# Performance work log

Hardware: AMD Instinct MI355X
Metric: run time of the kernel (lower is better)

Reference implementation:

```python
import jax, jax.numpy as jnp
import numpy as np

B, L, C, K, NLEV, VOCAB, OUT = 32, 1024, 512, 2, 4, 128, 11


def setup_inputs() -> dict:
    key = jax.random.key(0)
    ks = jax.random.split(key, 8)
    x = jax.random.randint(ks[0], (B, L), 0, VOCAB, dtype=jnp.int32)
    mask = jax.random.randint(ks[1], (B, L), 0, 2).astype(jnp.bool_)
    emb = jax.random.uniform(ks[2], (VOCAB, C), minval=-0.5, maxval=0.5, dtype=jnp.float32)
    w1 = jax.random.normal(ks[3], (NLEV, C, C, K), dtype=jnp.float32) * 0.02
    b1 = jnp.zeros((NLEV, C), dtype=jnp.float32)
    w2 = jax.random.normal(ks[4], (NLEV, C, C, K), dtype=jnp.float32) * 0.02
    b2 = jnp.zeros((NLEV, C), dtype=jnp.float32)
    dec_w = jax.random.uniform(ks[5], (OUT, C), minval=-0.5, maxval=0.5, dtype=jnp.float32)
    dec_b = jnp.zeros((OUT,), dtype=jnp.float32)
    return dict(x=x, mask=mask, emb=emb, w1=w1, b1=b1, w2=w2, b2=b2, dec_w=dec_w, dec_b=dec_b)


def _causal_conv(h, w, b, dilation):
    # h: [B, C, L], w: [Cout, Cin, K]; left-pad (K-1)*d == conv+chomp in TCN
    pad = (w.shape[-1] - 1) * dilation
    out = jax.lax.conv_general_dilated(
        h, w, window_strides=(1,), padding=[(pad, 0)],
        rhs_dilation=(dilation,), dimension_numbers=("NCH", "OIH", "NCH"))
    return out + b[None, :, None]


def reference(x, mask, emb, w1, b1, w2, b2, dec_w, dec_b):
    h = emb[x].transpose(0, 2, 1)  # [B, C, L]
    for i in range(NLEV):  # fixed small number of TCN levels
        d = 2 ** i
        res = h
        h = jax.nn.relu(_causal_conv(h, w1[i], b1[i], d))
        h = jax.nn.relu(_causal_conv(h, w2[i], b2[i], d))
        h = jax.nn.relu(h + res)  # residual (in==out channels -> identity shortcut)
    y = jnp.einsum("bcl,oc->blo", h, dec_w) + dec_b  # [B, L, OUT]
    # mask-gather: original keeps only mask-true positions; zero others (jit-safe)
    return y * mask[..., None].astype(y.dtype)
```

## Files before the change

### kernel.cpp

```cpp
#include <hip/hip_runtime.h>
#include <stdint.h>

#define BB 32
#define LL 1024
#define CC 512
#define NN (BB * LL)
#define NLEVS 4
#define OUTD 11
#define LPAD 8
#define LROWS (LL + LPAD)

typedef __attribute__((ext_vector_type(8))) short bf16x8;
typedef __attribute__((ext_vector_type(4))) float f32x4;

static __device__ __forceinline__ unsigned short f2bf(float f) {
    union { float f; uint32_t u; } v; v.f = f;
    uint32_t u = v.u;
    uint32_t r = (u + 0x7fffu + ((u >> 16) & 1u)) >> 16;
    return (unsigned short)r;
}
static __device__ __forceinline__ float bf2f(unsigned short h) {
    union { uint32_t u; float f; } v; v.u = ((uint32_t)h) << 16;
    return v.f;
}

static __device__ __forceinline__ void llds16(const unsigned short* g, unsigned short* l) {
    __builtin_amdgcn_global_load_lds(
        (const __attribute__((address_space(1))) unsigned int*)g,
        (__attribute__((address_space(3))) unsigned int*)l, 16, 0, 0);
}

__global__ __launch_bounds__(256) void prep_kernel(
    const int* __restrict__ x, const float* __restrict__ emb,
    const float* __restrict__ w1, const float* __restrict__ w2,
    const float* __restrict__ dw,
    unsigned short* __restrict__ Hb0, unsigned short* __restrict__ Hb1,
    unsigned short* __restrict__ WpT, unsigned short* __restrict__ dwp)
{
    int b = blockIdx.x;
    if (b < 16384) {
        int e = b * 256 + threadIdx.x;
        int cv = e >> 19;
        int r = e & 524287;
        int j = r >> 12;
        int co = (r >> 3) & 511;
        int h = r & 7;
        int kidx = j * 8 + h;
        int k = (kidx < 512) ? 1 : 0;
        int ci = kidx & 511;
        int lvl = cv >> 1;
        const float* w = (cv & 1) ? w2 : w1;
        WpT[e] = f2bf(w[(((size_t)(lvl * 512 + co) * 512) + ci) * 2 + k]);
    } else if (b < 24576) {
        int t = (b - 16384) * 256 + threadIdx.x;
        int n = t >> 6;
        int c8 = (t & 63) * 8;
        int idx = x[n];
        const float* src = emb + (size_t)idx * CC + c8;
        float4 v0 = *(const float4*)src;
        float4 v1 = *(const float4*)(src + 4);
        ushort4 a, bb;
        a.x = f2bf(v0.x); a.y = f2bf(v0.y); a.z = f2bf(v0.z); a.w = f2bf(v0.w);
        bb.x = f2bf(v1.x); bb.y = f2bf(v1.y); bb.z = f2bf(v1.z); bb.w = f2bf(v1.w);
        int prow = (n >> 10) * LROWS + LPAD + (n & (LL - 1));
        unsigned short* dst = Hb0 + (size_t)prow * CC + c8;
        *(ushort4*)dst = a;
        *(ushort4*)(dst + 4) = bb;
    } else if (b < 24704) {
        int t = (b - 24576) * 256 + threadIdx.x;
        unsigned short* base = (t >> 14) ? Hb1 : Hb0;
        int rem = t & 16383;
        int p = rem >> 9;
        int q = rem & 511;
        size_t off = (size_t)p * (LROWS * CC) + (size_t)q * 8;
        *(uint4*)(base + off) = (uint4){0u, 0u, 0u, 0u};
    } else {
        int e = (b - 24704) * 256 + threadIdx.x;
        int jb = e >> 7;
        int o = (e >> 3) & 15;
        int j = e & 7;
        dwp[e] = f2bf((o < OUTD) ? dw[o * CC + jb * 8 + j] : 0.f);
    }
}

#define PSEG 9
#define PBUFH (72 * 64)
template <bool HAS_RES>
__global__ __launch_bounds__(256, 4) void conv_gemm(
    const unsigned short* __restrict__ Ain, const unsigned short* __restrict__ WpT,
    const float* __restrict__ bias, const unsigned short* __restrict__ resB,
    unsigned short* __restrict__ OutB, int d)
{
    __shared__ unsigned short sA[2 * 2 * PBUFH];
    __shared__ int s_flag[4][8];

    const int tid = threadIdx.x;
    const int wave = tid >> 6, lane = tid & 63;
    const int pair = wave >> 1;

    const int bid = blockIdx.x;
    const int xcd = bid & 7;
    const int local = bid >> 3;
    const int cb = local >> 5;
    const int nb = xcd + 8 * (local & 31);
    const int co0 = cb * 128;
    const int n0 = nb * 128;

    const int rbase = (n0 >> 10) * LROWS + LPAD + (n0 & (LL - 1));
    const int wm = pair * 64;
    const int wn = (wave & 1) * 64;
    const int lm = lane & 15, quad = lane >> 4;

    const int r8 = lane >> 3;
    const int c8 = lane & 7;

    if (tid < 32) ((int*)s_flag)[tid] = 0;
    __syncthreads();

    f32x4 acc[4][4];
#pragma unroll
    for (int i = 0; i < 4; ++i)
#pragma unroll
        for (int j = 0; j < 4; ++j) acc[i][j] = (f32x4){0.f, 0.f, 0.f, 0.f};

    unsigned short* pb = sA + pair * (2 * PBUFH);
    const unsigned short* gAb =
        Ain + (size_t)(rbase - 8 + wm + r8) * CC + (c8 ^ r8) * 8;

    auto issue = [&](int it) {
        const unsigned short* gA = gAb + it * 64;
        unsigned short* lb = pb + (it & 1) * PBUFH;
#pragma unroll
        for (int seg = 0; seg < PSEG; ++seg)
            llds16(gA + (size_t)seg * 8 * CC, lb + seg * 512);
    };

    issue(0);

    for (int it = 0; it < 8; ++it) {
        if (it < 7) {
            if (it >= 1) {
                volatile int* vp = &s_flag[wave ^ 1][it - 1];
                while (*vp == 0) __builtin_amdgcn_s_sleep(1);
            }
            issue(it + 1);
            __builtin_amdgcn_s_waitcnt(0xF79);
        } else {
            __builtin_amdgcn_s_waitcnt(0xF70);
        }
        __asm__ volatile("" ::: "memory");

        const unsigned short* buf = pb + (it & 1) * PBUFH;
        const int jb0 = it * 8;

        auto loadA = [&](int s, bf16x8* af) {
            const int t = s >> 1, ks = s & 1;
            const int shift = t ? d : 0;
            const int rowoff = 8 - shift;
            const int key = (8 - shift + lm) & 7;
            const int cpos = ((ks * 4 + quad) ^ key);
#pragma unroll
            for (int mt = 0; mt < 4; ++mt)
                af[mt] = *(const bf16x8*)&buf[(rowoff + mt * 16 + lm) * 64 + cpos * 8];
        };
        auto loadB = [&](int s, bf16x8* bf) {
            const int t = s >> 1, ks = s & 1;
            const int jb = t * 64 + jb0 + ks * 4 + quad;
            const unsigned short* bbase = WpT + ((size_t)jb * 512 + co0 + wn + lm) * 8;
#pragma unroll
            for (int nt = 0; nt < 4; ++nt)
                bf[nt] = *(const bf16x8*)(bbase + (size_t)nt * 16 * 8);
        };

        bf16x8 afc[4], bfc[4], afn[4], bfn[4];
        loadA(0, afc);
        loadB(0, bfc);
#pragma unroll
        for (int s = 0; s < 4; ++s) {
            if (s < 3) { loadA(s + 1, afn); loadB(s + 1, bfn); }
#pragma unroll
            for (int mt = 0; mt < 4; ++mt)
#pragma unroll
                for (int nt = 0; nt < 4; ++nt)
                    acc[mt][nt] = __builtin_amdgcn_mfma_f32_16x16x32_bf16(
                        afc[mt], bfc[nt], acc[mt][nt], 0, 0, 0);
            if (s < 3) {
#pragma unroll
                for (int q2 = 0; q2 < 4; ++q2) { afc[q2] = afn[q2]; bfc[q2] = bfn[q2]; }
            }
        }

        __asm__ volatile("" ::: "memory");
        if (lane == 0) *(volatile int*)&s_flag[wave][it] = 1;
    }

    float bv[4];
#pragma unroll
    for (int nt = 0; nt < 4; ++nt) bv[nt] = bias[co0 + wn + nt * 16 + lm];

#pragma unroll
    for (int mt = 0; mt < 4; ++mt) {
        int prow0 = rbase + wm + mt * 16 + quad * 4;
#pragma unroll
        for (int nt = 0; nt < 4; ++nt) {
            int co = co0 + wn + nt * 16 + lm;
#pragma unroll
            for (int r = 0; r < 4; ++r) {
                size_t off = (size_t)(prow0 + r) * CC + co;
                float v = acc[mt][nt][r] + bv[nt];
                v = fmaxf(v, 0.f);
                if (HAS_RES) {
                    v += bf2f(resB[off]);
                    v = fmaxf(v, 0.f);
                }
                OutB[off] = f2bf(v);
            }
        }
    }
}

__global__ __launch_bounds__(256) void decode_kernel(
    const unsigned short* __restrict__ H, const unsigned short* __restrict__ dwp,
    const float* __restrict__ db, const int* __restrict__ mask,
    float* __restrict__ out)
{
    const int wave = threadIdx.x >> 6, lane = threadIdx.x & 63;
    const int lm = lane & 15, quad = lane >> 4;
    const int n0 = blockIdx.x * 64 + wave * 16;
    const int prow = ((n0 + lm) >> 10) * LROWS + LPAD + ((n0 + lm) & (LL - 1));

    f32x4 acc = (f32x4){0.f, 0.f, 0.f, 0.f};
#pragma unroll
    for (int ks = 0; ks < 16; ++ks) {
        bf16x8 af = *(const bf16x8*)&H[(size_t)prow * CC + ks * 32 + quad * 8];
        bf16x8 bf = *(const bf16x8*)&dwp[((size_t)(ks * 4 + quad) * 16 + lm) * 8];
        acc = __builtin_amdgcn_mfma_f32_16x16x32_bf16(af, bf, acc, 0, 0, 0);
    }

    if (lm < OUTD) {
        float bo = db[lm];
#pragma unroll
        for (int r = 0; r < 4; ++r) {
            int n = n0 + quad * 4 + r;
            float v = (mask[n] != 0) ? (acc[r] + bo) : 0.f;
            out[(size_t)n * OUTD + lm] = v;
        }
    }
}

extern "C" void kernel_launch(void* const* d_in, const int* in_sizes, int n_in,
                              void* d_out, int out_size, void* d_ws, size_t ws_size,
                              hipStream_t stream)
{
    const int* x = (const int*)d_in[0];
    const int* mask = (const int*)d_in[1];
    const float* emb = (const float*)d_in[2];
    const float* w1 = (const float*)d_in[3];
    const float* b1 = (const float*)d_in[4];
    const float* w2 = (const float*)d_in[5];
    const float* b2 = (const float*)d_in[6];
    const float* dw = (const float*)d_in[7];
    const float* db = (const float*)d_in[8];
    float* out = (float*)d_out;

    char* ws = (char*)d_ws;
    const size_t HBB = (size_t)BB * LROWS * CC * 2;
    unsigned short* Hb0 = (unsigned short*)ws;
    unsigned short* Hb1 = (unsigned short*)(ws + HBB);
    unsigned short* WpT = (unsigned short*)(ws + 2 * HBB);
    unsigned short* dwp = (unsigned short*)(ws + 2 * HBB + (size_t)NLEVS * 2 * CC * 1024 * 2);

    prep_kernel<<<24736, 256, 0, stream>>>(x, emb, w1, w2, dw, Hb0, Hb1, WpT, dwp);

    const int grid = (CC / 128) * (NN / 128);
    for (int i = 0; i < NLEVS; ++i) {
        int d = 1 << i;
        const unsigned short* W1 = WpT + (size_t)(i * 2 + 0) * CC * 1024;
        const unsigned short* W2 = WpT + (size_t)(i * 2 + 1) * CC * 1024;
        conv_gemm<false><<<grid, 256, 0, stream>>>(Hb0, W1, b1 + i * CC, nullptr, Hb1, d);
        conv_gemm<true><<<grid, 256, 0, stream>>>(Hb1, W2, b2 + i * CC, Hb0, Hb0, d);
    }
    decode_kernel<<<NN / 64, 256, 0, stream>>>(Hb0, dwp, db, mask, out);
}
```

Before: 413.4 us.

## Double the conv GEMM tile along positions and preload weights into registers

The conv GEMM block tile grows from 128 to 256 positions, so each wave computes 128x64 with 8x4 MFMA accumulators and the LDS staging buffer grows to 136 rows. All B-fragment (weight) loads for an iteration are issued into registers before the A-tile prefetch, which replaces the previous per-step software pipelining. The goal is to halve weight reloads per output and raise MFMA work per load. The cost is twice the accumulator registers and LDS, with occupancy cut from 4 to 2 blocks per CU and half as many blocks in the grid.

```diff
diff --git a/kernel.cpp b/kernel.cpp
--- a/kernel.cpp
+++ b/kernel.cpp
@@ -83,10 +83,11 @@
     }
 }
 
-#define PSEG 9
-#define PBUFH (72 * 64)
+#define PSEG 17
+#define SROWS 136
+#define PBUFH (SROWS * 64)
 template <bool HAS_RES>
-__global__ __launch_bounds__(256, 4) void conv_gemm(
+__global__ __launch_bounds__(256, 2) void conv_gemm(
     const unsigned short* __restrict__ Ain, const unsigned short* __restrict__ WpT,
     const float* __restrict__ bias, const unsigned short* __restrict__ resB,
     unsigned short* __restrict__ OutB, int d)
@@ -96,18 +97,18 @@
 
     const int tid = threadIdx.x;
     const int wave = tid >> 6, lane = tid & 63;
-    const int pair = wave >> 1;
+    const int pairi = wave >> 1;
 
     const int bid = blockIdx.x;
     const int xcd = bid & 7;
     const int local = bid >> 3;
-    const int cb = local >> 5;
-    const int nb = xcd + 8 * (local & 31);
+    const int cb = local >> 4;
+    const int nb = xcd + 8 * (local & 15);
     const int co0 = cb * 128;
-    const int n0 = nb * 128;
+    const int n0 = nb * 256;
 
     const int rbase = (n0 >> 10) * LROWS + LPAD + (n0 & (LL - 1));
-    const int wm = pair * 64;
+    const int wm = pairi * 128;
     const int wn = (wave & 1) * 64;
     const int lm = lane & 15, quad = lane >> 4;
 
@@ -117,13 +118,13 @@
     if (tid < 32) ((int*)s_flag)[tid] = 0;
     __syncthreads();
 
-    f32x4 acc[4][4];
-#pragma unroll
-    for (int i = 0; i < 4; ++i)
+    f32x4 acc[8][4];
+#pragma unroll
+    for (int i = 0; i < 8; ++i)
 #pragma unroll
         for (int j = 0; j < 4; ++j) acc[i][j] = (f32x4){0.f, 0.f, 0.f, 0.f};
 
-    unsigned short* pb = sA + pair * (2 * PBUFH);
+    unsigned short* pb = sA + pairi * (2 * PBUFH);
     const unsigned short* gAb =
         Ain + (size_t)(rbase - 8 + wm + r8) * CC + (c8 ^ r8) * 8;
 
@@ -137,56 +138,56 @@
 
     issue(0);
 
+    bf16x8 breg[4][4];
+
     for (int it = 0; it < 8; ++it) {
+        __builtin_amdgcn_s_waitcnt(0xF70);
+        __asm__ volatile("" ::: "memory");
+
+        const int jb0 = it * 8;
+#pragma unroll
+        for (int s = 0; s < 4; ++s) {
+            const int t = s >> 1, ks = s & 1;
+            const int jb = t * 64 + jb0 + ks * 4 + quad;
+            const unsigned short* bbase = WpT + ((size_t)jb * 512 + co0 + wn + lm) * 8;
+#pragma unroll
+            for (int nt = 0; nt < 4; ++nt)
+                breg[s][nt] = *(const bf16x8*)(bbase + (size_t)nt * 16 * 8);
+        }
+        __asm__ volatile("" ::: "memory");
+
         if (it < 7) {
             if (it >= 1) {
                 volatile int* vp = &s_flag[wave ^ 1][it - 1];
                 while (*vp == 0) __builtin_amdgcn_s_sleep(1);
             }
             issue(it + 1);
-            __builtin_amdgcn_s_waitcnt(0xF79);
-        } else {
-            __builtin_amdgcn_s_waitcnt(0xF70);
         }
         __asm__ volatile("" ::: "memory");
 
         const unsigned short* buf = pb + (it & 1) * PBUFH;
-        const int jb0 = it * 8;
-
-        auto loadA = [&](int s, bf16x8* af) {
+
+#pragma unroll
+        for (int s = 0; s < 4; ++s) {
             const int t = s >> 1, ks = s & 1;
             const int shift = t ? d : 0;
             const int rowoff = 8 - shift;
             const int key = (8 - shift + lm) & 7;
             const int cpos = ((ks * 4 + quad) ^ key);
 #pragma unroll
-            for (int mt = 0; mt < 4; ++mt)
-                af[mt] = *(const bf16x8*)&buf[(rowoff + mt * 16 + lm) * 64 + cpos * 8];
-        };
-        auto loadB = [&](int s, bf16x8* bf) {
-            const int t = s >> 1, ks = s & 1;
-            const int jb = t * 64 + jb0 + ks * 4 + quad;
-            const unsigned short* bbase = WpT + ((size_t)jb * 512 + co0 + wn + lm) * 8;
-#pragma unroll
-            for (int nt = 0; nt < 4; ++nt)
-                bf[nt] = *(const bf16x8*)(bbase + (size_t)nt * 16 * 8);
-        };
-
-        bf16x8 afc[4], bfc[4], afn[4], bfn[4];
-        loadA(0, afc);
-        loadB(0, bfc);
-#pragma unroll
-        for (int s = 0; s < 4; ++s) {
-            if (s < 3) { loadA(s + 1, afn); loadB(s + 1, bfn); }
-#pragma unroll
-            for (int mt = 0; mt < 4; ++mt)
-#pragma unroll
-                for (int nt = 0; nt < 4; ++nt)
-                    acc[mt][nt] = __builtin_amdgcn_mfma_f32_16x16x32_bf16(
-                        afc[mt], bfc[nt], acc[mt][nt], 0, 0, 0);
-            if (s < 3) {
-#pragma unroll
-                for (int q2 = 0; q2 < 4; ++q2) { afc[q2] = afn[q2]; bfc[q2] = bfn[q2]; }
+            for (int half = 0; half < 2; ++half) {
+                bf16x8 af[4];
+#pragma unroll
+                for (int q = 0; q < 4; ++q) {
+                    const int mt = half * 4 + q;
+                    af[q] = *(const bf16x8*)&buf[(rowoff + mt * 16 + lm) * 64 + cpos * 8];
+                }
+#pragma unroll
+                for (int q = 0; q < 4; ++q)
+#pragma unroll
+                    for (int nt = 0; nt < 4; ++nt)
+                        acc[half * 4 + q][nt] = __builtin_amdgcn_mfma_f32_16x16x32_bf16(
+                            af[q], breg[s][nt], acc[half * 4 + q][nt], 0, 0, 0);
             }
         }
 
@@ -199,7 +200,7 @@
     for (int nt = 0; nt < 4; ++nt) bv[nt] = bias[co0 + wn + nt * 16 + lm];
 
 #pragma unroll
-    for (int mt = 0; mt < 4; ++mt) {
+    for (int mt = 0; mt < 8; ++mt) {
         int prow0 = rbase + wm + mt * 16 + quad * 4;
 #pragma unroll
         for (int nt = 0; nt < 4; ++nt) {
@@ -272,7 +273,7 @@
 
     prep_kernel<<<24736, 256, 0, stream>>>(x, emb, w1, w2, dw, Hb0, Hb1, WpT, dwp);
 
-    const int grid = (CC / 128) * (NN / 128);
+    const int grid = (CC / 128) * (NN / 256);
     for (int i = 0; i < NLEVS; ++i) {
         int d = 1 << i;
         const unsigned short* W1 = WpT + (size_t)(i * 2 + 0) * CC * 1024;
```

Result: faster. 393.5 us, median of 2 (-4.8%).
